# Kernel optimization log

Hardware: AMD Instinct MI355X
Metric: run time of the kernel (lower is better)

Reference implementation:

```python
import jax, jax.numpy as jnp
import numpy as np

N_NODES = 100000
N_EDGES = 1600000
IN_CH, HID_CH, OUT_CH = 128, 128, 64
N_GRAPHS = 64


def gcn_conv(x, src, dst, W, b, n_nodes):
    """PyG-style GCNConv: self-loops already included in (src, dst).
    out_i = b + sum_j norm_ij * (x_j @ W), norm_ij = deg_i^-1/2 * deg_j^-1/2."""
    xw = x @ W  # [N, out]
    deg = jax.ops.segment_sum(jnp.ones_like(dst, dtype=xw.dtype), dst,
                              num_segments=n_nodes)  # [N]
    dinv = jnp.where(deg > 0, jax.lax.rsqrt(jnp.maximum(deg, 1e-12)), 0.0)
    norm = dinv[src] * dinv[dst]  # [E]
    msg = xw[src] * norm[:, None]  # gather + scale  [E, out]
    out = jax.ops.segment_sum(msg, dst, num_segments=n_nodes)  # scatter-add
    return out + b


def global_mean_pool(x, batch, n_graphs):
    s = jax.ops.segment_sum(x, batch, num_segments=n_graphs)
    cnt = jax.ops.segment_sum(jnp.ones((x.shape[0],), x.dtype), batch,
                              num_segments=n_graphs)
    return s / jnp.maximum(cnt, 1.0)[:, None]


def setup_inputs() -> dict:
    key = jax.random.key(0)
    ks = jax.random.split(key, 9)
    x = jax.random.normal(ks[0], (N_NODES, IN_CH), dtype=jnp.float32)
    edge_index = jax.random.randint(ks[1], (2, N_EDGES), 0, N_NODES, dtype=jnp.int64)
    batch = jnp.sort(jax.random.randint(ks[2], (N_NODES,), 0, N_GRAPHS, dtype=jnp.int64))
    # Glorot-ish params
    s1 = 1.0 / np.sqrt(IN_CH)
    s2 = 1.0 / np.sqrt(HID_CH)
    W1 = jax.random.normal(ks[3], (IN_CH, HID_CH), jnp.float32) * s1
    b1 = jnp.zeros((HID_CH,), jnp.float32)
    W2 = jax.random.normal(ks[4], (HID_CH, HID_CH), jnp.float32) * s2
    b2 = jnp.zeros((HID_CH,), jnp.float32)
    Wl = jax.random.normal(ks[5], (HID_CH, OUT_CH), jnp.float32) * s2
    bl = jax.random.normal(ks[6], (OUT_CH,), jnp.float32) * 0.01
    return {"x": x, "edge_index": edge_index, "batch": batch,
            "W1": W1, "b1": b1, "W2": W2, "b2": b2, "Wl": Wl, "bl": bl}


def reference(x, edge_index, batch, W1, b1, W2, b2, Wl, bl):
    n = x.shape[0]
    loop = jnp.arange(n, dtype=edge_index.dtype)
    src = jnp.concatenate([edge_index[0], loop])  # add self-loops
    dst = jnp.concatenate([edge_index[1], loop])
    h = jax.nn.relu(gcn_conv(x, src, dst, W1, b1, n))
    h = jax.nn.relu(gcn_conv(h, src, dst, W2, b2, n))
    g = global_mean_pool(h, batch, N_GRAPHS)  # [B, hid]
    return g @ Wl + bl  # [B, out]
```

## Files before the change

kernel.cpp:

```cpp
#include <hip/hip_runtime.h>

#define N_NODESC 100000
#define N_EDGESC 1600000
#define CH 128
#define NG 64
#define OC 64

#define GST_BLKS 391
#define MFMA_BLKS 1563
#define PAD_STRIDE 64
#define SENTINEL N_NODESC

#define BIN_SHIFT 9
#define BIN_W 512
#define NBINS 196
#define BIN_CAP 16384
#define BIN1_BLKS 391
#define E_PER_BIN1 4096

#define K0_BLKS (BIN1_BLKS + 64 + GST_BLKS + MFMA_BLKS)

typedef __attribute__((ext_vector_type(8))) short short8;
typedef __attribute__((ext_vector_type(4))) float f32x4;

__device__ __forceinline__ unsigned short f2b_u(float f) {
    union { float f; unsigned int u; } x; x.f = f;
    unsigned int u = x.u;
    return (unsigned short)((u + 0x7fffu + ((u >> 16) & 1u)) >> 16);
}

#define WSTR 136
template<int AFP, int DM>
__device__ __forceinline__ void mfma_compute(int blk, int t, const void* __restrict__ Ap,
                                             signed char* __restrict__ Oq,
                                             float* __restrict__ osc,
                                             const float* __restrict__ dmul,
                                             const unsigned short* WsT) {
    int wave = t >> 6, lane = t & 63;
    int quad = lane >> 4, l16 = lane & 15;
    int arow = blk * 64 + wave * 16 + l16;
    bool rowok = arow < N_NODESC;
    f32x4 acc[8] = {};
#pragma unroll
    for (int c = 0; c < 4; ++c) {
        int koff = c * 32 + quad * 8;
        short8 a;
        if (AFP) {
            const float* A = (const float*)Ap;
            float4 f0 = make_float4(0, 0, 0, 0), f1 = make_float4(0, 0, 0, 0);
            if (rowok) {
                f0 = *(const float4*)(A + (size_t)arow * 128 + koff);
                f1 = *(const float4*)(A + (size_t)arow * 128 + koff + 4);
            }
            a[0] = (short)f2b_u(f0.x); a[1] = (short)f2b_u(f0.y);
            a[2] = (short)f2b_u(f0.z); a[3] = (short)f2b_u(f0.w);
            a[4] = (short)f2b_u(f1.x); a[5] = (short)f2b_u(f1.y);
            a[6] = (short)f2b_u(f1.z); a[7] = (short)f2b_u(f1.w);
        } else {
            const unsigned short* A = (const unsigned short*)Ap;
            if (rowok) a = *(const short8*)(A + (size_t)arow * 128 + koff);
            else       a = (short8)(short)0;
        }
#pragma unroll
        for (int tt = 0; tt < 8; ++tt) {
            short8 b = *(const short8*)&WsT[(tt * 16 + l16) * WSTR + koff];
            acc[tt] = __builtin_amdgcn_mfma_f32_16x16x32_bf16(a, b, acc[tt], 0, 0, 0);
        }
    }
    int orow0 = blk * 64 + wave * 16 + quad * 4;
#pragma unroll
    for (int r = 0; r < 4; ++r) {
        int g = orow0 + r;
        float m = 0.f;
#pragma unroll
        for (int tt = 0; tt < 8; ++tt) m = fmaxf(m, fabsf(acc[tt][r]));
        m = fmaxf(m, __shfl_xor(m, 1));
        m = fmaxf(m, __shfl_xor(m, 2));
        m = fmaxf(m, __shfl_xor(m, 4));
        m = fmaxf(m, __shfl_xor(m, 8));
        float inv = m > 0.f ? 127.f / m : 0.f;
        if (g < N_NODESC) {
#pragma unroll
            for (int tt = 0; tt < 8; ++tt)
                Oq[(size_t)g * 128 + tt * 16 + l16] = (signed char)(int)rintf(acc[tt][r] * inv);
            if (l16 == 0) {
                float s = m * (1.f / 127.f);
                osc[g] = DM ? dmul[g] * s : s;
            }
        }
    }
}

__global__ __launch_bounds__(256) void k_pre(const int* __restrict__ ei,
                                             const int* __restrict__ batch,
                                             const float* __restrict__ W1,
                                             const float* __restrict__ W2,
                                             int* __restrict__ cursor,
                                             unsigned int* __restrict__ binbuf,
                                             unsigned short* __restrict__ Wt2,
                                             int* __restrict__ gstart,
                                             float* __restrict__ xsc,
                                             const float* __restrict__ x,
                                             signed char* __restrict__ xwq) {
    __shared__ unsigned short WsT[128 * WSTR];
    int b = blockIdx.x, t = threadIdx.x;
    if (b < BIN1_BLKS) {
        int* hist = (int*)WsT;
        for (int i = t; i < NBINS; i += 256) hist[i] = 0;
        __syncthreads();
        int e0 = b * E_PER_BIN1;
#pragma unroll 4
        for (int i = 0; i < E_PER_BIN1 / 256; ++i) {
            int e = e0 + i * 256 + t;
            if (e < N_EDGESC) atomicAdd(&hist[ei[N_EDGESC + e] >> BIN_SHIFT], 1);
        }
        __syncthreads();
        for (int i = t; i < NBINS; i += 256) {
            int c = hist[i];
            hist[i] = c ? atomicAdd(&cursor[i], c) : 0;
        }
        __syncthreads();
#pragma unroll 4
        for (int i = 0; i < E_PER_BIN1 / 256; ++i) {
            int e = e0 + i * 256 + t;
            if (e < N_EDGESC) {
                int d = ei[N_EDGESC + e];
                int s = ei[e];
                int bin = d >> BIN_SHIFT;
                int off = atomicAdd(&hist[bin], 1);
                binbuf[(size_t)bin * BIN_CAP + off] =
                    ((unsigned int)(d & (BIN_W - 1)) << 17) | (unsigned int)s;
            }
        }
    } else if (b < BIN1_BLKS + 64) {
        int i = (b - BIN1_BLKS) * 256 + t;
        int k = i >> 7, c = i & 127;
        Wt2[c * 128 + k] = f2b_u(W2[k * 128 + c]);
    } else if (b < BIN1_BLKS + 64 + GST_BLKS) {
        int i = (b - BIN1_BLKS - 64) * 256 + t;
        if (i >= N_NODESC) {
            if (i == N_NODESC) xsc[SENTINEL] = 0.f;
            return;
        }
        int bb = batch[i];
        int bp = (i == 0) ? -1 : batch[i - 1];
        for (int g = bp + 1; g <= bb; ++g) gstart[g] = i;
        if (i == N_NODESC - 1)
            for (int g = bb + 1; g <= NG; ++g) gstart[g] = N_NODESC;
    } else {
        int blk = b - (BIN1_BLKS + 64 + GST_BLKS);
        for (int idx = t; idx < 16384; idx += 256) {
            int k = idx >> 7, c = idx & 127;
            WsT[c * WSTR + k] = f2b_u(W1[idx]);
        }
        __syncthreads();
        mfma_compute<1, 0>(blk, t, x, xwq, xsc, nullptr, WsT);
    }
}

__global__ __launch_bounds__(256) void k_bin2(const int* __restrict__ cursor,
                                              const unsigned int* __restrict__ binbuf,
                                              const float* __restrict__ xsc,
                                              int* __restrict__ deg,
                                              float* __restrict__ dinvt,
                                              float* __restrict__ wsc,
                                              int* __restrict__ pad) {
    __shared__ int ldeg[BIN_W];
    int bin = blockIdx.x, t = threadIdx.x;
    if (bin == 0 && t == 0) { dinvt[SENTINEL] = 0.f; wsc[SENTINEL] = 0.f; }
    for (int i = t; i < BIN_W; i += 256) ldeg[i] = 0;
    __syncthreads();
    int n = cursor[bin];
    size_t base = (size_t)bin * BIN_CAP;
    for (int i = t; i < n; i += 256) {
        unsigned int rec = binbuf[base + i];
        int dl = rec >> 17;
        int s = rec & 0x1FFFF;
        int slot = atomicAdd(&ldeg[dl], 1) & (PAD_STRIDE - 1);
        pad[(size_t)((bin << BIN_SHIFT) + dl) * PAD_STRIDE + slot] = s;
    }
    __syncthreads();
    for (int i = t; i < BIN_W; i += 256) {
        int node = (bin << BIN_SHIFT) + i;
        if (node < N_NODESC) {
            int dg = ldeg[i];
            if (dg > PAD_STRIDE) dg = PAD_STRIDE;
            deg[node] = dg;
            float dv = rsqrtf((float)(dg + 1));
            dinvt[node] = dv;
            wsc[node] = dv * xsc[node];
            int r8 = (dg + 7) & ~7;
            for (int j = dg; j < r8; ++j)
                pad[(size_t)node * PAD_STRIDE + j] = SENTINEL;
        }
    }
}

__global__ __launch_bounds__(256) void k_mfma2(const unsigned short* __restrict__ A,
                                               const unsigned short* __restrict__ Wt,
                                               signed char* __restrict__ Oq,
                                               float* __restrict__ wsc,
                                               const float* __restrict__ dinvt) {
    __shared__ unsigned short WsT[128 * WSTR];
    int t = threadIdx.x;
    {
        const uint4* wsrc = (const uint4*)Wt;
        for (int idx = t; idx < 2048; idx += 256) {
            int row = idx >> 4, sub = idx & 15;
            *((uint4*)&WsT[row * WSTR] + sub) = wsrc[row * 16 + sub];
        }
    }
    __syncthreads();
    mfma_compute<0, 1>(blockIdx.x, t, A, Oq, wsc, dinvt, WsT);
}

__device__ __forceinline__ void accq(float* acc, unsigned int lo, unsigned int hi, float wk) {
    acc[0] += wk * (float)((int)(lo << 24) >> 24);
    acc[1] += wk * (float)((int)(lo << 16) >> 24);
    acc[2] += wk * (float)((int)(lo <<  8) >> 24);
    acc[3] += wk * (float)((int)lo >> 24);
    acc[4] += wk * (float)((int)(hi << 24) >> 24);
    acc[5] += wk * (float)((int)(hi << 16) >> 24);
    acc[6] += wk * (float)((int)(hi <<  8) >> 24);
    acc[7] += wk * (float)((int)hi >> 24);
}

__device__ __forceinline__ void accum8(const signed char* __restrict__ xwq,
                                       const float* __restrict__ wsc,
                                       const int4* __restrict__ prow,
                                       int kb, int l16, float* acc) {
    int4 p0 = prow[kb * 2], p1 = prow[kb * 2 + 1];
    int s[8] = {p0.x, p0.y, p0.z, p0.w, p1.x, p1.y, p1.z, p1.w};
    float w[8];
    uint2 v[8];
#pragma unroll
    for (int k = 0; k < 8; ++k) {
        w[k] = wsc[s[k]];
        v[k] = *(const uint2*)&xwq[(size_t)(unsigned int)s[k] * 128 + l16 * 8];
    }
#pragma unroll
    for (int k = 0; k < 8; ++k) accq(acc, v[k].x, v[k].y, w[k]);
}

__device__ __forceinline__ void gather_pair(const signed char* __restrict__ xwq,
                                            const float* __restrict__ wsc,
                                            const int* __restrict__ pad,
                                            int nA, int nB, int nbA, int nbB,
                                            int l16, float* accA, float* accB) {
    const int4* prA = (const int4*)&pad[nA * PAD_STRIDE];
    const int4* prB = (const int4*)&pad[nB * PAD_STRIDE];
    int nmax = nbA > nbB ? nbA : nbB;
    for (int kb = 0; kb < nmax; ++kb) {
        if (kb < nbA) accum8(xwq, wsc, prA, kb, l16, accA);
        if (kb < nbB) accum8(xwq, wsc, prB, kb, l16, accB);
    }
}

__global__ __launch_bounds__(256) void k_gather1(const signed char* __restrict__ xwq,
                                                 const float* __restrict__ wsc,
                                                 const int* __restrict__ deg,
                                                 const float* __restrict__ dinvt,
                                                 const int* __restrict__ pad,
                                                 const float* __restrict__ bias,
                                                 unsigned int* __restrict__ outp) {
    int t = threadIdx.x;
    int lane = t & 63, w = t >> 6;
    int g = lane >> 4, l16 = lane & 15;
    int nA = blockIdx.x * 32 + w * 8 + g * 2;
    int nB = nA + 1;
    int dgA = deg[nA], dgB = deg[nB];
    float wnA = dinvt[nA], wnB = dinvt[nB];
    float wsA = wsc[nA], wsB = wsc[nB];
    uint2 vsA = *(const uint2*)&xwq[(size_t)(unsigned int)nA * 128 + l16 * 8];
    uint2 vsB = *(const uint2*)&xwq[(size_t)(unsigned int)nB * 128 + l16 * 8];
    float accA[8] = {0.f, 0.f, 0.f, 0.f, 0.f, 0.f, 0.f, 0.f};
    float accB[8] = {0.f, 0.f, 0.f, 0.f, 0.f, 0.f, 0.f, 0.f};
    accq(accA, vsA.x, vsA.y, wsA);
    accq(accB, vsB.x, vsB.y, wsB);
    gather_pair(xwq, wsc, pad, nA, nB, (dgA + 7) >> 3, (dgB + 7) >> 3, l16, accA, accB);
    float4 bA = *(const float4*)&bias[l16 * 8];
    float4 bB = *(const float4*)&bias[l16 * 8 + 4];
    float oA[8], oB[8];
    oA[0] = fmaxf(bA.x + wnA * accA[0], 0.f); oA[1] = fmaxf(bA.y + wnA * accA[1], 0.f);
    oA[2] = fmaxf(bA.z + wnA * accA[2], 0.f); oA[3] = fmaxf(bA.w + wnA * accA[3], 0.f);
    oA[4] = fmaxf(bB.x + wnA * accA[4], 0.f); oA[5] = fmaxf(bB.y + wnA * accA[5], 0.f);
    oA[6] = fmaxf(bB.z + wnA * accA[6], 0.f); oA[7] = fmaxf(bB.w + wnA * accA[7], 0.f);
    oB[0] = fmaxf(bA.x + wnB * accB[0], 0.f); oB[1] = fmaxf(bA.y + wnB * accB[1], 0.f);
    oB[2] = fmaxf(bA.z + wnB * accB[2], 0.f); oB[3] = fmaxf(bA.w + wnB * accB[3], 0.f);
    oB[4] = fmaxf(bB.x + wnB * accB[4], 0.f); oB[5] = fmaxf(bB.y + wnB * accB[5], 0.f);
    oB[6] = fmaxf(bB.z + wnB * accB[6], 0.f); oB[7] = fmaxf(bB.w + wnB * accB[7], 0.f);
    uint4 ovA, ovB;
    ovA.x = ((unsigned int)f2b_u(oA[1]) << 16) | (unsigned int)f2b_u(oA[0]);
    ovA.y = ((unsigned int)f2b_u(oA[3]) << 16) | (unsigned int)f2b_u(oA[2]);
    ovA.z = ((unsigned int)f2b_u(oA[5]) << 16) | (unsigned int)f2b_u(oA[4]);
    ovA.w = ((unsigned int)f2b_u(oA[7]) << 16) | (unsigned int)f2b_u(oA[6]);
    ovB.x = ((unsigned int)f2b_u(oB[1]) << 16) | (unsigned int)f2b_u(oB[0]);
    ovB.y = ((unsigned int)f2b_u(oB[3]) << 16) | (unsigned int)f2b_u(oB[2]);
    ovB.z = ((unsigned int)f2b_u(oB[5]) << 16) | (unsigned int)f2b_u(oB[4]);
    ovB.w = ((unsigned int)f2b_u(oB[7]) << 16) | (unsigned int)f2b_u(oB[6]);
    *(uint4*)&outp[(unsigned int)nA * 64 + l16 * 4] = ovA;
    *(uint4*)&outp[(unsigned int)nB * 64 + l16 * 4] = ovB;
}

__global__ __launch_bounds__(256) void k_gather_pool(const signed char* __restrict__ xwq,
                                                     const float* __restrict__ wsc,
                                                     const int* __restrict__ deg,
                                                     const float* __restrict__ dinvt,
                                                     const int* __restrict__ pad,
                                                     const float* __restrict__ bias,
                                                     const int* __restrict__ batch,
                                                     float* __restrict__ gpart) {
    __shared__ float lds[4 * 128];
    int t = threadIdx.x, w = t >> 6, lane = t & 63;
    int g = lane >> 4, l16 = lane & 15;
    int base = blockIdx.x * 32;
    int nA = base + w * 8 + g * 2;
    int nB = nA + 1;
    int dgA = deg[nA], dgB = deg[nB];
    float wnA = dinvt[nA], wnB = dinvt[nB];
    float wsA = wsc[nA], wsB = wsc[nB];
    uint2 vsA = *(const uint2*)&xwq[(size_t)(unsigned int)nA * 128 + l16 * 8];
    uint2 vsB = *(const uint2*)&xwq[(size_t)(unsigned int)nB * 128 + l16 * 8];
    float accA[8] = {0.f, 0.f, 0.f, 0.f, 0.f, 0.f, 0.f, 0.f};
    float accB[8] = {0.f, 0.f, 0.f, 0.f, 0.f, 0.f, 0.f, 0.f};
    accq(accA, vsA.x, vsA.y, wsA);
    accq(accB, vsB.x, vsB.y, wsB);
    gather_pair(xwq, wsc, pad, nA, nB, (dgA + 7) >> 3, (dgB + 7) >> 3, l16, accA, accB);
    float4 bA = *(const float4*)&bias[l16 * 8];
    float4 bB = *(const float4*)&bias[l16 * 8 + 4];
    float oA[8], oB[8];
    oA[0] = fmaxf(bA.x + wnA * accA[0], 0.f); oA[1] = fmaxf(bA.y + wnA * accA[1], 0.f);
    oA[2] = fmaxf(bA.z + wnA * accA[2], 0.f); oA[3] = fmaxf(bA.w + wnA * accA[3], 0.f);
    oA[4] = fmaxf(bB.x + wnA * accA[4], 0.f); oA[5] = fmaxf(bB.y + wnA * accA[5], 0.f);
    oA[6] = fmaxf(bB.z + wnA * accA[6], 0.f); oA[7] = fmaxf(bB.w + wnA * accA[7], 0.f);
    oB[0] = fmaxf(bA.x + wnB * accB[0], 0.f); oB[1] = fmaxf(bA.y + wnB * accB[1], 0.f);
    oB[2] = fmaxf(bA.z + wnB * accB[2], 0.f); oB[3] = fmaxf(bA.w + wnB * accB[3], 0.f);
    oB[4] = fmaxf(bB.x + wnB * accB[4], 0.f); oB[5] = fmaxf(bB.y + wnB * accB[5], 0.f);
    oB[6] = fmaxf(bB.z + wnB * accB[6], 0.f); oB[7] = fmaxf(bB.w + wnB * accB[7], 0.f);
    bool fast = batch[base] == batch[base + 31];
    if (fast) {
#pragma unroll
        for (int j = 0; j < 8; ++j) {
            float v = oA[j] + oB[j];
            v += __shfl_xor(v, 16);
            v += __shfl_xor(v, 32);
            oA[j] = v;
        }
        if (lane < 16) {
#pragma unroll
            for (int j = 0; j < 8; ++j) lds[w * 128 + l16 * 8 + j] = oA[j];
        }
        __syncthreads();
        if (t < 128) {
            float v = lds[t] + lds[128 + t] + lds[256 + t] + lds[384 + t];
            atomicAdd(&gpart[batch[base] * 128 + t], v);
        }
    } else {
        int gA = batch[nA], gB = batch[nB];
#pragma unroll
        for (int j = 0; j < 8; ++j) {
            atomicAdd(&gpart[gA * 128 + l16 * 8 + j], oA[j]);
            atomicAdd(&gpart[gB * 128 + l16 * 8 + j], oB[j]);
        }
    }
}

__global__ void k_final(const float* __restrict__ gpart, const int* __restrict__ gstart,
                        const float* __restrict__ Wl, const float* __restrict__ bl,
                        float* __restrict__ out) {
    __shared__ float gs[128];
    int b = blockIdx.x;
    int o = threadIdx.x;
    gs[o] = gpart[b * 128 + o];
    gs[o + 64] = gpart[b * 128 + 64 + o];
    __syncthreads();
    int cnt = gstart[b + 1] - gstart[b];
    float sc = 1.f / (float)(cnt > 0 ? cnt : 1);
    float sum = 0.f;
    for (int k = 0; k < 128; ++k) sum += gs[k] * Wl[k * 64 + o];
    out[b * 64 + o] = bl[o] + sc * sum;
}

extern "C" void kernel_launch(void* const* d_in, const int* in_sizes, int n_in,
                              void* d_out, int out_size, void* d_ws, size_t ws_size,
                              hipStream_t stream) {
    const float* x    = (const float*)d_in[0];
    const int*   ei   = (const int*)d_in[1];
    const int*   batch= (const int*)d_in[2];
    const float* W1   = (const float*)d_in[3];
    const float* b1   = (const float*)d_in[4];
    const float* W2   = (const float*)d_in[5];
    const float* b2   = (const float*)d_in[6];
    const float* Wl   = (const float*)d_in[7];
    const float* bl   = (const float*)d_in[8];
    float* out = (float*)d_out;

    char* ws = (char*)d_ws;
    signed char* xwq = (signed char*)ws; ws += (size_t)(N_NODESC + 1) * CH;
    unsigned short* h_b = (unsigned short*)ws; ws += (size_t)N_NODESC * CH * 2;
    unsigned short* Wt2 = (unsigned short*)ws; ws += (size_t)CH * CH * 2;
    int*   cursor = (int*)ws;   ws += (size_t)NBINS * 4;
    float* gpart  = (float*)ws; ws += (size_t)NG * CH * 4;
    int*   deg    = (int*)ws;   ws += (size_t)N_NODESC * 4;
    float* dinvt  = (float*)ws; ws += (size_t)(N_NODESC + 4) * 4;
    float* xsc    = (float*)ws; ws += (size_t)(N_NODESC + 4) * 4;
    float* wsc    = (float*)ws; ws += (size_t)(N_NODESC + 4) * 4;
    int*   pad    = (int*)ws;   ws += (size_t)N_NODESC * PAD_STRIDE * 4;
    unsigned int* binbuf = (unsigned int*)ws; ws += (size_t)NBINS * BIN_CAP * 4;
    int*   gstart = (int*)ws;   ws += (NG + 8) * 4;

    hipMemsetAsync(cursor, 0, (size_t)NBINS * 4 + (size_t)NG * CH * 4, stream);

    k_pre<<<K0_BLKS, 256, 0, stream>>>(ei, batch, W1, W2, cursor, binbuf,
                                       Wt2, gstart, xsc, x, xwq);
    k_bin2<<<NBINS, 256, 0, stream>>>(cursor, binbuf, xsc, deg, dinvt, wsc, pad);

    k_gather1<<<N_NODESC / 32, 256, 0, stream>>>(xwq, wsc, deg, dinvt, pad, b1,
                                                 (unsigned int*)h_b);
    k_mfma2<<<MFMA_BLKS, 256, 0, stream>>>(h_b, Wt2, xwq, wsc, dinvt);
    k_gather_pool<<<N_NODESC / 32, 256, 0, stream>>>(xwq, wsc, deg, dinvt, pad, b2,
                                                     batch, gpart);

    k_final<<<NG, 64, 0, stream>>>(gpart, gstart, Wl, bl, out);
}
```

Before: 282.2 us.

## Fuse layer-1 gather with layer-2 MFMA transform through shared memory

Merges the first-layer neighbor gather (bias+ReLU) with the second-layer bf16 MFMA matmul into one kernel. Each block gathers 64 node rows into LDS as bf16, then multiplies by W2 from LDS and writes int8-quantized output with per-row scales to a separate buffer. This removes the bf16 hidden-state round trip through global memory and one kernel launch. In exchange each block now does both a latency-bound gather and an MFMA phase, which may change occupancy because of the larger LDS footprint and fewer nodes per wave.

Measured after the change: 292.4 us. +3.6%, slower.

```diff
diff --git a/kernel.cpp b/kernel.cpp
--- a/kernel.cpp
+++ b/kernel.cpp
@@ -8,6 +8,7 @@
 
 #define GST_BLKS 391
 #define MFMA_BLKS 1563
+#define G1M2_BLKS 1563
 #define PAD_STRIDE 64
 #define SENTINEL N_NODESC
 
@@ -164,10 +165,13 @@
                                               int* __restrict__ deg,
                                               float* __restrict__ dinvt,
                                               float* __restrict__ wsc,
+                                              float* __restrict__ wsc2,
                                               int* __restrict__ pad) {
     __shared__ int ldeg[BIN_W];
     int bin = blockIdx.x, t = threadIdx.x;
-    if (bin == 0 && t == 0) { dinvt[SENTINEL] = 0.f; wsc[SENTINEL] = 0.f; }
+    if (bin == 0 && t == 0) {
+        dinvt[SENTINEL] = 0.f; wsc[SENTINEL] = 0.f; wsc2[SENTINEL] = 0.f;
+    }
     for (int i = t; i < BIN_W; i += 256) ldeg[i] = 0;
     __syncthreads();
     int n = cursor[bin];
@@ -196,24 +200,6 @@
     }
 }
 
-__global__ __launch_bounds__(256) void k_mfma2(const unsigned short* __restrict__ A,
-                                               const unsigned short* __restrict__ Wt,
-                                               signed char* __restrict__ Oq,
-                                               float* __restrict__ wsc,
-                                               const float* __restrict__ dinvt) {
-    __shared__ unsigned short WsT[128 * WSTR];
-    int t = threadIdx.x;
-    {
-        const uint4* wsrc = (const uint4*)Wt;
-        for (int idx = t; idx < 2048; idx += 256) {
-            int row = idx >> 4, sub = idx & 15;
-            *((uint4*)&WsT[row * WSTR] + sub) = wsrc[row * 16 + sub];
-        }
-    }
-    __syncthreads();
-    mfma_compute<0, 1>(blockIdx.x, t, A, Oq, wsc, dinvt, WsT);
-}
-
 __device__ __forceinline__ void accq(float* acc, unsigned int lo, unsigned int hi, float wk) {
     acc[0] += wk * (float)((int)(lo << 24) >> 24);
     acc[1] += wk * (float)((int)(lo << 16) >> 24);
@@ -256,18 +242,14 @@
     }
 }
 
-__global__ __launch_bounds__(256) void k_gather1(const signed char* __restrict__ xwq,
+__device__ __forceinline__ void gather_relu_pair(const signed char* __restrict__ xwq,
                                                  const float* __restrict__ wsc,
                                                  const int* __restrict__ deg,
                                                  const float* __restrict__ dinvt,
                                                  const int* __restrict__ pad,
                                                  const float* __restrict__ bias,
-                                                 unsigned int* __restrict__ outp) {
-    int t = threadIdx.x;
-    int lane = t & 63, w = t >> 6;
-    int g = lane >> 4, l16 = lane & 15;
-    int nA = blockIdx.x * 32 + w * 8 + g * 2;
-    int nB = nA + 1;
+                                                 int nA, int nB, int l16,
+                                                 float* oA, float* oB) {
     int dgA = deg[nA], dgB = deg[nB];
     float wnA = dinvt[nA], wnB = dinvt[nB];
     float wsA = wsc[nA], wsB = wsc[nB];
@@ -280,7 +262,6 @@
     gather_pair(xwq, wsc, pad, nA, nB, (dgA + 7) >> 3, (dgB + 7) >> 3, l16, accA, accB);
     float4 bA = *(const float4*)&bias[l16 * 8];
     float4 bB = *(const float4*)&bias[l16 * 8 + 4];
-    float oA[8], oB[8];
     oA[0] = fmaxf(bA.x + wnA * accA[0], 0.f); oA[1] = fmaxf(bA.y + wnA * accA[1], 0.f);
     oA[2] = fmaxf(bA.z + wnA * accA[2], 0.f); oA[3] = fmaxf(bA.w + wnA * accA[3], 0.f);
     oA[4] = fmaxf(bB.x + wnA * accA[4], 0.f); oA[5] = fmaxf(bB.y + wnA * accA[5], 0.f);
@@ -289,17 +270,82 @@
     oB[2] = fmaxf(bA.z + wnB * accB[2], 0.f); oB[3] = fmaxf(bA.w + wnB * accB[3], 0.f);
     oB[4] = fmaxf(bB.x + wnB * accB[4], 0.f); oB[5] = fmaxf(bB.y + wnB * accB[5], 0.f);
     oB[6] = fmaxf(bB.z + wnB * accB[6], 0.f); oB[7] = fmaxf(bB.w + wnB * accB[7], 0.f);
-    uint4 ovA, ovB;
-    ovA.x = ((unsigned int)f2b_u(oA[1]) << 16) | (unsigned int)f2b_u(oA[0]);
-    ovA.y = ((unsigned int)f2b_u(oA[3]) << 16) | (unsigned int)f2b_u(oA[2]);
-    ovA.z = ((unsigned int)f2b_u(oA[5]) << 16) | (unsigned int)f2b_u(oA[4]);
-    ovA.w = ((unsigned int)f2b_u(oA[7]) << 16) | (unsigned int)f2b_u(oA[6]);
-    ovB.x = ((unsigned int)f2b_u(oB[1]) << 16) | (unsigned int)f2b_u(oB[0]);
-    ovB.y = ((unsigned int)f2b_u(oB[3]) << 16) | (unsigned int)f2b_u(oB[2]);
-    ovB.z = ((unsigned int)f2b_u(oB[5]) << 16) | (unsigned int)f2b_u(oB[4]);
-    ovB.w = ((unsigned int)f2b_u(oB[7]) << 16) | (unsigned int)f2b_u(oB[6]);
-    *(uint4*)&outp[(unsigned int)nA * 64 + l16 * 4] = ovA;
-    *(uint4*)&outp[(unsigned int)nB * 64 + l16 * 4] = ovB;
+}
+
+__device__ __forceinline__ uint4 pack_bf16x8(const float* o) {
+    uint4 ov;
+    ov.x = ((unsigned int)f2b_u(o[1]) << 16) | (unsigned int)f2b_u(o[0]);
+    ov.y = ((unsigned int)f2b_u(o[3]) << 16) | (unsigned int)f2b_u(o[2]);
+    ov.z = ((unsigned int)f2b_u(o[5]) << 16) | (unsigned int)f2b_u(o[4]);
+    ov.w = ((unsigned int)f2b_u(o[7]) << 16) | (unsigned int)f2b_u(o[6]);
+    return ov;
+}
+
+__global__ __launch_bounds__(256) void k_g1m2(const signed char* __restrict__ xwq,
+                                              const float* __restrict__ wsc,
+                                              const int* __restrict__ deg,
+                                              const float* __restrict__ dinvt,
+                                              const int* __restrict__ pad,
+                                              const float* __restrict__ bias,
+                                              const unsigned short* __restrict__ Wt2,
+                                              signed char* __restrict__ xwq2,
+                                              float* __restrict__ wsc2) {
+    __shared__ unsigned short WsT[128 * WSTR];
+    __shared__ unsigned short Hs[64 * WSTR];
+    int t = threadIdx.x, w = t >> 6, lane = t & 63;
+    int g = lane >> 4, l16 = lane & 15;
+    {
+        const uint4* wsrc = (const uint4*)Wt2;
+        for (int idx = t; idx < 2048; idx += 256) {
+            int row = idx >> 4, sub = idx & 15;
+            *((uint4*)&WsT[row * WSTR] + sub) = wsrc[row * 16 + sub];
+        }
+    }
+    int base = blockIdx.x * 64;
+#pragma unroll
+    for (int p = 0; p < 2; ++p) {
+        int nA = base + w * 16 + p * 8 + g * 2;
+        int nB = nA + 1;
+        if (nA < N_NODESC) {
+            float oA[8], oB[8];
+            gather_relu_pair(xwq, wsc, deg, dinvt, pad, bias, nA, nB, l16, oA, oB);
+            *(uint4*)&Hs[(nA - base) * WSTR + l16 * 8] = pack_bf16x8(oA);
+            *(uint4*)&Hs[(nB - base) * WSTR + l16 * 8] = pack_bf16x8(oB);
+        }
+    }
+    __syncthreads();
+    int quad = g;
+    f32x4 acc[8] = {};
+    const unsigned short* Arow = &Hs[(w * 16 + l16) * WSTR];
+#pragma unroll
+    for (int c = 0; c < 4; ++c) {
+        int koff = c * 32 + quad * 8;
+        short8 a = *(const short8*)&Arow[koff];
+#pragma unroll
+        for (int tt = 0; tt < 8; ++tt) {
+            short8 b = *(const short8*)&WsT[(tt * 16 + l16) * WSTR + koff];
+            acc[tt] = __builtin_amdgcn_mfma_f32_16x16x32_bf16(a, b, acc[tt], 0, 0, 0);
+        }
+    }
+    int orow0 = base + w * 16 + quad * 4;
+#pragma unroll
+    for (int r = 0; r < 4; ++r) {
+        int gg = orow0 + r;
+        float m = 0.f;
+#pragma unroll
+        for (int tt = 0; tt < 8; ++tt) m = fmaxf(m, fabsf(acc[tt][r]));
+        m = fmaxf(m, __shfl_xor(m, 1));
+        m = fmaxf(m, __shfl_xor(m, 2));
+        m = fmaxf(m, __shfl_xor(m, 4));
+        m = fmaxf(m, __shfl_xor(m, 8));
+        float inv = m > 0.f ? 127.f / m : 0.f;
+        if (gg < N_NODESC) {
+#pragma unroll
+            for (int tt = 0; tt < 8; ++tt)
+                xwq2[(size_t)gg * 128 + tt * 16 + l16] = (signed char)(int)rintf(acc[tt][r] * inv);
+            if (l16 == 0) wsc2[gg] = dinvt[gg] * (m * (1.f / 127.f));
+        }
+    }
 }
 
 __global__ __launch_bounds__(256) void k_gather_pool(const signed char* __restrict__ xwq,
@@ -316,27 +362,8 @@
     int base = blockIdx.x * 32;
     int nA = base + w * 8 + g * 2;
     int nB = nA + 1;
-    int dgA = deg[nA], dgB = deg[nB];
-    float wnA = dinvt[nA], wnB = dinvt[nB];
-    float wsA = wsc[nA], wsB = wsc[nB];
-    uint2 vsA = *(const uint2*)&xwq[(size_t)(unsigned int)nA * 128 + l16 * 8];
-    uint2 vsB = *(const uint2*)&xwq[(size_t)(unsigned int)nB * 128 + l16 * 8];
-    float accA[8] = {0.f, 0.f, 0.f, 0.f, 0.f, 0.f, 0.f, 0.f};
-    float accB[8] = {0.f, 0.f, 0.f, 0.f, 0.f, 0.f, 0.f, 0.f};
-    accq(accA, vsA.x, vsA.y, wsA);
-    accq(accB, vsB.x, vsB.y, wsB);
-    gather_pair(xwq, wsc, pad, nA, nB, (dgA + 7) >> 3, (dgB + 7) >> 3, l16, accA, accB);
-    float4 bA = *(const float4*)&bias[l16 * 8];
-    float4 bB = *(const float4*)&bias[l16 * 8 + 4];
     float oA[8], oB[8];
-    oA[0] = fmaxf(bA.x + wnA * accA[0], 0.f); oA[1] = fmaxf(bA.y + wnA * accA[1], 0.f);
-    oA[2] = fmaxf(bA.z + wnA * accA[2], 0.f); oA[3] = fmaxf(bA.w + wnA * accA[3], 0.f);
-    oA[4] = fmaxf(bB.x + wnA * accA[4], 0.f); oA[5] = fmaxf(bB.y + wnA * accA[5], 0.f);
-    oA[6] = fmaxf(bB.z + wnA * accA[6], 0.f); oA[7] = fmaxf(bB.w + wnA * accA[7], 0.f);
-    oB[0] = fmaxf(bA.x + wnB * accB[0], 0.f); oB[1] = fmaxf(bA.y + wnB * accB[1], 0.f);
-    oB[2] = fmaxf(bA.z + wnB * accB[2], 0.f); oB[3] = fmaxf(bA.w + wnB * accB[3], 0.f);
-    oB[4] = fmaxf(bB.x + wnB * accB[4], 0.f); oB[5] = fmaxf(bB.y + wnB * accB[5], 0.f);
-    oB[6] = fmaxf(bB.z + wnB * accB[6], 0.f); oB[7] = fmaxf(bB.w + wnB * accB[7], 0.f);
+    gather_relu_pair(xwq, wsc, deg, dinvt, pad, bias, nA, nB, l16, oA, oB);
     bool fast = batch[base] == batch[base + 31];
     if (fast) {
 #pragma unroll
@@ -396,8 +423,8 @@
     float* out = (float*)d_out;
 
     char* ws = (char*)d_ws;
-    signed char* xwq = (signed char*)ws; ws += (size_t)(N_NODESC + 1) * CH;
-    unsigned short* h_b = (unsigned short*)ws; ws += (size_t)N_NODESC * CH * 2;
+    signed char* xwq  = (signed char*)ws; ws += (size_t)(N_NODESC + 1) * CH;
+    signed char* xwq2 = (signed char*)ws; ws += (size_t)(N_NODESC + 1) * CH;
     unsigned short* Wt2 = (unsigned short*)ws; ws += (size_t)CH * CH * 2;
     int*   cursor = (int*)ws;   ws += (size_t)NBINS * 4;
     float* gpart  = (float*)ws; ws += (size_t)NG * CH * 4;
@@ -405,6 +432,7 @@
     float* dinvt  = (float*)ws; ws += (size_t)(N_NODESC + 4) * 4;
     float* xsc    = (float*)ws; ws += (size_t)(N_NODESC + 4) * 4;
     float* wsc    = (float*)ws; ws += (size_t)(N_NODESC + 4) * 4;
+    float* wsc2   = (float*)ws; ws += (size_t)(N_NODESC + 4) * 4;
     int*   pad    = (int*)ws;   ws += (size_t)N_NODESC * PAD_STRIDE * 4;
     unsigned int* binbuf = (unsigned int*)ws; ws += (size_t)NBINS * BIN_CAP * 4;
     int*   gstart = (int*)ws;   ws += (NG + 8) * 4;
@@ -413,12 +441,11 @@
 
     k_pre<<<K0_BLKS, 256, 0, stream>>>(ei, batch, W1, W2, cursor, binbuf,
                                        Wt2, gstart, xsc, x, xwq);
-    k_bin2<<<NBINS, 256, 0, stream>>>(cursor, binbuf, xsc, deg, dinvt, wsc, pad);
-
-    k_gather1<<<N_NODESC / 32, 256, 0, stream>>>(xwq, wsc, deg, dinvt, pad, b1,
-                                                 (unsigned int*)h_b);
-    k_mfma2<<<MFMA_BLKS, 256, 0, stream>>>(h_b, Wt2, xwq, wsc, dinvt);
-    k_gather_pool<<<N_NODESC / 32, 256, 0, stream>>>(xwq, wsc, deg, dinvt, pad, b2,
+    k_bin2<<<NBINS, 256, 0, stream>>>(cursor, binbuf, xsc, deg, dinvt, wsc, wsc2, pad);
+
+    k_g1m2<<<G1M2_BLKS, 256, 0, stream>>>(xwq, wsc, deg, dinvt, pad, b1,
+                                          Wt2, xwq2, wsc2);
+    k_gather_pool<<<N_NODESC / 32, 256, 0, stream>>>(xwq2, wsc2, deg, dinvt, pad, b2,
                                                      batch, gpart);
 
     k_final<<<NG, 64, 0, stream>>>(gpart, gstart, Wl, bl, out);
```
